# Kernel optimization log

Measured on AMD Instinct MI355X. Metric: run time of the kernel, lower is better.

## Reference

```python
import jax, jax.numpy as jnp
import numpy as np

NEG_FILL = -10000.0  # matches masked_fill_(mask, -10000.0)


def setup_inputs() -> dict:
    key0 = jax.random.key(0)
    kq, kk, kv, km = jax.random.split(key0, 4)
    B, H, S, D = 2, 16, 2048, 64
    query = jax.random.normal(kq, (B, H, S, D), dtype=jnp.float32)
    key = jax.random.normal(kk, (B, H, S, D), dtype=jnp.float32)
    value = jax.random.normal(kv, (B, H, S, D), dtype=jnp.float32)
    # key-padding mask [B, S]; True = position is masked out
    mask = jax.random.randint(km, (B, S), 0, 2).astype(jnp.bool_)
    return {"query": query, "key": key, "value": value, "mask": mask}


def reference(query, key, value, mask):
    # scaled dot-product attention: [B,H,S,D] x [B,H,S,D] -> [B,H,S,S]
    scale = 1.0 / jnp.sqrt(jnp.asarray(query.shape[-1], query.dtype))
    scores = jnp.einsum('bhqd,bhkd->bhqk', query, key) * scale
    # mask [B,S] -> broadcast over heads and query positions as [B,1,1,S]
    scores = jnp.where(mask[:, None, None, :], jnp.asarray(NEG_FILL, scores.dtype), scores)
    attn = jax.nn.softmax(scores, axis=-1)
    # dropout probs are 0 (eval-mode identity)
    out = jnp.einsum('bhqk,bhkd->bhqd', attn, value)
    return out
```

## Files before the change

### kernel.cpp

```cpp
#include <hip/hip_runtime.h>
#include <hip/hip_bf16.h>
#include <stdint.h>

namespace {

constexpr int Bb = 2;
constexpr int Hh = 16;
constexpr int Ss = 2048;
constexpr int Dd = 64;
constexpr int KT = 64;
constexpr int NT = Ss / KT;
constexpr int TILE_BYTES = KT * Dd * 2;
constexpr int BH_BYTES = NT * TILE_BYTES;
constexpr size_t KPRE_BYTES = (size_t)Bb * Hh * Ss * Dd * 2;
constexpr size_t VPRE_OFF = KPRE_BYTES;
constexpr size_t MASK_OFF = 2 * KPRE_BYTES;
constexpr size_t WS_NEED = MASK_OFF + (size_t)Bb * NT * 8;

typedef __bf16 bf16x8 __attribute__((ext_vector_type(8)));
typedef float floatx4 __attribute__((ext_vector_type(4)));

typedef __attribute__((address_space(1))) const unsigned int guint;
typedef __attribute__((address_space(3))) unsigned int luint;

__device__ __forceinline__ void g2lds16(const void* g, void* l) {
  __builtin_amdgcn_global_load_lds((guint*)g, (luint*)l, 16, 0, 0);
}

__global__ __launch_bounds__(256) void preprocess4(
    const float* __restrict__ K, const float* __restrict__ V,
    const int* __restrict__ mask, uint8_t* __restrict__ ws)
{
  const int tid = threadIdx.x;
  const int kt = blockIdx.x;
  const int bh = blockIdx.y;

  if (blockIdx.z == 0) {
    const int c = tid & 7;
#pragma unroll
    for (int half = 0; half < 2; ++half) {
      const int row = (tid >> 3) + half * 32;
      const float4* src = (const float4*)(K + ((size_t)bh * 2048 + kt * 64 + row) * 64 + c * 8);
      const float4 a = src[0], b2 = src[1];
      bf16x8 pk;
      pk[0] = (__bf16)a.x;  pk[1] = (__bf16)a.y;  pk[2] = (__bf16)a.z;  pk[3] = (__bf16)a.w;
      pk[4] = (__bf16)b2.x; pk[5] = (__bf16)b2.y; pk[6] = (__bf16)b2.z; pk[7] = (__bf16)b2.w;
      uint8_t* dst = ws + (size_t)bh * BH_BYTES + kt * TILE_BYTES + row * 128 + ((c ^ (row & 7)) << 4);
      *(bf16x8*)dst = pk;
    }
    if (bh == 0 && kt < 16) {
      const int i = kt * 256 + tid;
      const int bb = i >> 11, key = i & 2047;
      const unsigned long long bal = __ballot(mask[bb * 2048 + key] != 0);
      if ((key & 63) == 0)
        ((unsigned long long*)(ws + MASK_OFF))[bb * NT + (key >> 6)] = bal;
    }
    return;
  }

  const int d2  = tid & 31;
  const int c16 = tid >> 5;
  const int s2 = c16 & 1, q = c16 >> 1;
  const int k0 = 32 * s2 + 4 * q;
  const float* vbase = V + ((size_t)bh * 2048 + kt * 64) * 64;
  float2 col[8];
#pragma unroll
  for (int j = 0; j < 4; ++j) {
    col[j]     = *(const float2*)(vbase + (size_t)(k0 + j) * 64 + 2 * d2);
    col[4 + j] = *(const float2*)(vbase + (size_t)(k0 + 16 + j) * 64 + 2 * d2);
  }
#pragma unroll
  for (int h = 0; h < 2; ++h) {
    const int d = 2 * d2 + h;
    bf16x8 pv;
#pragma unroll
    for (int j = 0; j < 4; ++j) {
      pv[j]     = (__bf16)(h ? col[j].y     : col[j].x);
      pv[4 + j] = (__bf16)(h ? col[4 + j].y : col[4 + j].x);
    }
    uint8_t* dst = ws + VPRE_OFF + (size_t)bh * BH_BYTES + kt * TILE_BYTES + d * 128 + ((c16 ^ (d & 7)) << 4);
    *(bf16x8*)dst = pv;
  }
}

#define NEGM (-14426.950408889634f)
#define MFMA16 __builtin_amdgcn_mfma_f32_16x16x32_bf16

__global__ __launch_bounds__(256, 2) void attn_fused9(
    const float* __restrict__ Q, const uint8_t* __restrict__ ws,
    float* __restrict__ Out)
{
  const int tid  = threadIdx.x;
  const int wave = tid >> 6;
  const int lane = tid & 63;
  const int ln   = lane & 15;
  const int quad = lane >> 4;

  const int bh   = blockIdx.x;
  const int qblk = blockIdx.y;
  const int b    = bh >> 4;

  const float* Qb = Q + (size_t)bh * Ss * Dd;
  float*       Ob = Out + (size_t)bh * Ss * Dd;
  const uint8_t* Kpre = ws + (size_t)bh * BH_BYTES;
  const uint8_t* Vpre = ws + VPRE_OFF + (size_t)bh * BH_BYTES;
  const unsigned long long* Mbits = (const unsigned long long*)(ws + MASK_OFF) + b * NT;

  __shared__ __align__(16) __bf16 Klds[2][64 * Dd];
  __shared__ __align__(16) __bf16 Vlds[2][64 * Dd];

  const int q0A = qblk * 128 + wave * 32;
  const int q0B = q0A + 16;

  const float QS = 0.125f * 1.44269504088896340736f;
  bf16x8 aqA0, aqA1, aqB0, aqB1;
  {
    const float* qpA = Qb + (size_t)(q0A + ln) * Dd + quad * 8;
    const float* qpB = Qb + (size_t)(q0B + ln) * Dd + quad * 8;
#pragma unroll
    for (int j = 0; j < 8; ++j) {
      aqA0[j] = (__bf16)(qpA[j] * QS);
      aqA1[j] = (__bf16)(qpA[32 + j] * QS);
      aqB0[j] = (__bf16)(qpB[j] * QS);
      aqB1[j] = (__bf16)(qpB[32 + j] * QS);
    }
  }

  floatx4 oA[4], oB[4];
  floatx4 laccA = (floatx4){0.f, 0.f, 0.f, 0.f};
  floatx4 laccB = (floatx4){0.f, 0.f, 0.f, 0.f};
#pragma unroll
  for (int nd = 0; nd < 4; ++nd) {
    oA[nd] = (floatx4){0.f, 0.f, 0.f, 0.f};
    oB[nd] = (floatx4){0.f, 0.f, 0.f, 0.f};
  }

  const int swz0 = (quad ^ (ln & 7)) << 4;
  const int swz1 = ((quad + 4) ^ (ln & 7)) << 4;
  const int soff = wave * 1024 + lane * 16;

  g2lds16(Kpre + soff,        (uint8_t*)Klds[0] + soff);
  g2lds16(Kpre + soff + 4096, (uint8_t*)Klds[0] + soff + 4096);
  g2lds16(Vpre + soff,        (uint8_t*)Vlds[0] + soff);
  g2lds16(Vpre + soff + 4096, (uint8_t*)Vlds[0] + soff + 4096);

  for (int it = 0; it < NT; ++it) {
    const int cur = it & 1;
    __syncthreads();

    if (it + 1 < NT) {
      const uint8_t* kg = Kpre + (it + 1) * TILE_BYTES;
      const uint8_t* vg = Vpre + (it + 1) * TILE_BYTES;
      uint8_t* kl = (uint8_t*)Klds[cur ^ 1];
      uint8_t* vl = (uint8_t*)Vlds[cur ^ 1];
      g2lds16(kg + soff,        kl + soff);
      g2lds16(kg + soff + 4096, kl + soff + 4096);
      g2lds16(vg + soff,        vl + soff);
      g2lds16(vg + soff + 4096, vl + soff + 4096);
    }

    const unsigned long long mb = Mbits[it];

    const uint8_t* Kb = (const uint8_t*)Klds[cur];
    const uint8_t* Vb = (const uint8_t*)Vlds[cur];

    auto loadK = [&](int sub, bf16x8& b0, bf16x8& b1) {
      const uint8_t* krow = Kb + (sub * 16 + ln) * 128;
      b0 = *(const bf16x8*)(krow + swz0);
      b1 = *(const bf16x8*)(krow + swz1);
    };
    auto loadV = [&](int s2, bf16x8* w) {
#pragma unroll
      for (int nd = 0; nd < 4; ++nd) {
        const uint8_t* vrow = Vb + (nd * 16 + ln) * 128;
        w[nd] = *(const bf16x8*)(vrow + (((quad * 2 + s2) ^ (ln & 7)) << 4));
      }
    };

    __builtin_amdgcn_s_setprio(1);

    bf16x8 kf0[2][2], kf1[2][2];
    bf16x8 vf[2][4];
    loadK(0, kf0[0][0], kf1[0][0]);
    loadK(1, kf0[0][1], kf1[0][1]);
    loadV(0, vf[0]);

#pragma unroll
    for (int p = 0; p < 2; ++p) {
      if (p == 0) {
        loadK(2, kf0[1][0], kf1[1][0]);
        loadK(3, kf0[1][1], kf1[1][1]);
        loadV(1, vf[1]);
      }

      const uint32_t bits0 = (uint32_t)(mb >> ((2 * p) * 16 + quad * 4));
      const uint32_t bits1 = (uint32_t)(mb >> ((2 * p + 1) * 16 + quad * 4));
      floatx4 sA0, sA1, sB0, sB1;
#pragma unroll
      for (int r = 0; r < 4; ++r) {
        const float b0v = ((bits0 >> r) & 1) ? NEGM : 0.f;
        const float b1v = ((bits1 >> r) & 1) ? NEGM : 0.f;
        sA0[r] = b0v; sB0[r] = b0v;
        sA1[r] = b1v; sB1[r] = b1v;
      }

      sA0 = MFMA16(kf0[p][0], aqA0, sA0, 0, 0, 0);
      sA0 = MFMA16(kf1[p][0], aqA1, sA0, 0, 0, 0);
      sB0 = MFMA16(kf0[p][0], aqB0, sB0, 0, 0, 0);
      sB0 = MFMA16(kf1[p][0], aqB1, sB0, 0, 0, 0);
      sA1 = MFMA16(kf0[p][1], aqA0, sA1, 0, 0, 0);
      sA1 = MFMA16(kf1[p][1], aqA1, sA1, 0, 0, 0);
      sB1 = MFMA16(kf0[p][1], aqB0, sB1, 0, 0, 0);
      sB1 = MFMA16(kf1[p][1], aqB1, sB1, 0, 0, 0);

      bf16x8 bpA, bpB;
#pragma unroll
      for (int r = 0; r < 4; ++r) {
        const float pA0 = __builtin_amdgcn_exp2f(sA0[r]);
        const float pA1 = __builtin_amdgcn_exp2f(sA1[r]);
        const float pB0 = __builtin_amdgcn_exp2f(sB0[r]);
        const float pB1 = __builtin_amdgcn_exp2f(sB1[r]);
        laccA[r] += pA0 + pA1;
        laccB[r] += pB0 + pB1;
        bpA[r] = (__bf16)pA0; bpA[4 + r] = (__bf16)pA1;
        bpB[r] = (__bf16)pB0; bpB[4 + r] = (__bf16)pB1;
      }

#pragma unroll
      for (int nd = 0; nd < 4; ++nd) {
        oA[nd] = MFMA16(vf[p][nd], bpA, oA[nd], 0, 0, 0);
        oB[nd] = MFMA16(vf[p][nd], bpB, oB[nd], 0, 0, 0);
      }
    }
    __builtin_amdgcn_s_setprio(0);
  }

  float lA = (laccA[0] + laccA[1]) + (laccA[2] + laccA[3]);
  float lB = (laccB[0] + laccB[1]) + (laccB[2] + laccB[3]);
  lA += __shfl_xor(lA, 16); lA += __shfl_xor(lA, 32);
  lB += __shfl_xor(lB, 16); lB += __shfl_xor(lB, 32);
  const float iA = 1.0f / lA, iB = 1.0f / lB;
#pragma unroll
  for (int nd = 0; nd < 4; ++nd) {
    float4 wv;
    wv.x = oA[nd][0] * iA; wv.y = oA[nd][1] * iA;
    wv.z = oA[nd][2] * iA; wv.w = oA[nd][3] * iA;
    *(float4*)(Ob + (size_t)(q0A + ln) * Dd + nd * 16 + quad * 4) = wv;
    wv.x = oB[nd][0] * iB; wv.y = oB[nd][1] * iB;
    wv.z = oB[nd][2] * iB; wv.w = oB[nd][3] * iB;
    *(float4*)(Ob + (size_t)(q0B + ln) * Dd + nd * 16 + quad * 4) = wv;
  }
}

}

extern "C" void kernel_launch(void* const* d_in, const int* in_sizes, int n_in,
                              void* d_out, int out_size, void* d_ws, size_t ws_size,
                              hipStream_t stream) {
  const float* Q   = (const float*)d_in[0];
  const float* K   = (const float*)d_in[1];
  const float* V   = (const float*)d_in[2];
  const int*  mask = (const int*)d_in[3];
  float* Out = (float*)d_out;

  preprocess4<<<dim3(32, 32, 2), 256, 0, stream>>>(K, V, mask, (uint8_t*)d_ws);
  attn_fused9<<<dim3(Bb * Hh, Ss / 128), 256, 0, stream>>>(Q, (const uint8_t*)d_ws, Out);
  (void)ws_size; (void)in_sizes; (void)n_in; (void)out_size;
}
```

Measured before the change: 139.0 us.

## Replace LDS double-buffering with direct global-to-register K/V prefetch

Removes the shared-memory staging of K/V tiles and the per-iteration __syncthreads, loading MFMA fragments straight from the pre-swizzled workspace in global memory. The next tile's first-half fragments are prefetched into registers during the second half of the current tile. The aim is to drop barrier and LDS traffic costs so waves run independently. In exchange each wave re-fetches K/V from L2/global, raising cache bandwidth demand and exposing global latency.

```diff
diff --git a/kernel.cpp b/kernel.cpp
--- a/kernel.cpp
+++ b/kernel.cpp
@@ -15,17 +15,9 @@
 constexpr size_t KPRE_BYTES = (size_t)Bb * Hh * Ss * Dd * 2;
 constexpr size_t VPRE_OFF = KPRE_BYTES;
 constexpr size_t MASK_OFF = 2 * KPRE_BYTES;
-constexpr size_t WS_NEED = MASK_OFF + (size_t)Bb * NT * 8;
 
 typedef __bf16 bf16x8 __attribute__((ext_vector_type(8)));
 typedef float floatx4 __attribute__((ext_vector_type(4)));
-
-typedef __attribute__((address_space(1))) const unsigned int guint;
-typedef __attribute__((address_space(3))) unsigned int luint;
-
-__device__ __forceinline__ void g2lds16(const void* g, void* l) {
-  __builtin_amdgcn_global_load_lds((guint*)g, (luint*)l, 16, 0, 0);
-}
 
 __global__ __launch_bounds__(256) void preprocess4(
     const float* __restrict__ K, const float* __restrict__ V,
@@ -86,7 +78,7 @@
 #define NEGM (-14426.950408889634f)
 #define MFMA16 __builtin_amdgcn_mfma_f32_16x16x32_bf16
 
-__global__ __launch_bounds__(256, 2) void attn_fused9(
+__global__ __launch_bounds__(256, 2) void attn_fused10(
     const float* __restrict__ Q, const uint8_t* __restrict__ ws,
     float* __restrict__ Out)
 {
@@ -106,9 +98,6 @@
   const uint8_t* Vpre = ws + VPRE_OFF + (size_t)bh * BH_BYTES;
   const unsigned long long* Mbits = (const unsigned long long*)(ws + MASK_OFF) + b * NT;
 
-  __shared__ __align__(16) __bf16 Klds[2][64 * Dd];
-  __shared__ __align__(16) __bf16 Vlds[2][64 * Dd];
-
   const int q0A = qblk * 128 + wave * 32;
   const int q0B = q0A + 16;
 
@@ -137,60 +126,42 @@
 
   const int swz0 = (quad ^ (ln & 7)) << 4;
   const int swz1 = ((quad + 4) ^ (ln & 7)) << 4;
-  const int soff = wave * 1024 + lane * 16;
-
-  g2lds16(Kpre + soff,        (uint8_t*)Klds[0] + soff);
-  g2lds16(Kpre + soff + 4096, (uint8_t*)Klds[0] + soff + 4096);
-  g2lds16(Vpre + soff,        (uint8_t*)Vlds[0] + soff);
-  g2lds16(Vpre + soff + 4096, (uint8_t*)Vlds[0] + soff + 4096);
+  const int vsw0 = ((quad * 2 + 0) ^ (ln & 7)) << 4;
+  const int vsw1 = ((quad * 2 + 1) ^ (ln & 7)) << 4;
+
+  auto loadK = [&](const uint8_t* Kb, int sub, bf16x8& b0, bf16x8& b1) {
+    const uint8_t* krow = Kb + (sub * 16 + ln) * 128;
+    b0 = *(const bf16x8*)(krow + swz0);
+    b1 = *(const bf16x8*)(krow + swz1);
+  };
+  auto loadV = [&](const uint8_t* Vb, int s2, bf16x8* w) {
+    const int vsw = s2 ? vsw1 : vsw0;
+#pragma unroll
+    for (int nd = 0; nd < 4; ++nd)
+      w[nd] = *(const bf16x8*)(Vb + (nd * 16 + ln) * 128 + vsw);
+  };
+
+  bf16x8 kf0[2][2], kf1[2][2];
+  bf16x8 vf[2][4];
+  loadK(Kpre, 0, kf0[0][0], kf1[0][0]);
+  loadK(Kpre, 1, kf0[0][1], kf1[0][1]);
+  loadV(Vpre, 0, vf[0]);
 
   for (int it = 0; it < NT; ++it) {
-    const int cur = it & 1;
-    __syncthreads();
-
-    if (it + 1 < NT) {
-      const uint8_t* kg = Kpre + (it + 1) * TILE_BYTES;
-      const uint8_t* vg = Vpre + (it + 1) * TILE_BYTES;
-      uint8_t* kl = (uint8_t*)Klds[cur ^ 1];
-      uint8_t* vl = (uint8_t*)Vlds[cur ^ 1];
-      g2lds16(kg + soff,        kl + soff);
-      g2lds16(kg + soff + 4096, kl + soff + 4096);
-      g2lds16(vg + soff,        vl + soff);
-      g2lds16(vg + soff + 4096, vl + soff + 4096);
-    }
-
+    const uint8_t* Kb = Kpre + it * TILE_BYTES;
+    const uint8_t* Vb = Vpre + it * TILE_BYTES;
     const unsigned long long mb = Mbits[it];
-
-    const uint8_t* Kb = (const uint8_t*)Klds[cur];
-    const uint8_t* Vb = (const uint8_t*)Vlds[cur];
-
-    auto loadK = [&](int sub, bf16x8& b0, bf16x8& b1) {
-      const uint8_t* krow = Kb + (sub * 16 + ln) * 128;
-      b0 = *(const bf16x8*)(krow + swz0);
-      b1 = *(const bf16x8*)(krow + swz1);
-    };
-    auto loadV = [&](int s2, bf16x8* w) {
-#pragma unroll
-      for (int nd = 0; nd < 4; ++nd) {
-        const uint8_t* vrow = Vb + (nd * 16 + ln) * 128;
-        w[nd] = *(const bf16x8*)(vrow + (((quad * 2 + s2) ^ (ln & 7)) << 4));
-      }
-    };
-
-    __builtin_amdgcn_s_setprio(1);
-
-    bf16x8 kf0[2][2], kf1[2][2];
-    bf16x8 vf[2][4];
-    loadK(0, kf0[0][0], kf1[0][0]);
-    loadK(1, kf0[0][1], kf1[0][1]);
-    loadV(0, vf[0]);
 
 #pragma unroll
     for (int p = 0; p < 2; ++p) {
       if (p == 0) {
-        loadK(2, kf0[1][0], kf1[1][0]);
-        loadK(3, kf0[1][1], kf1[1][1]);
-        loadV(1, vf[1]);
+        loadK(Kb, 2, kf0[1][0], kf1[1][0]);
+        loadK(Kb, 3, kf0[1][1], kf1[1][1]);
+        loadV(Vb, 1, vf[1]);
+      } else if (it + 1 < NT) {
+        loadK(Kb + TILE_BYTES, 0, kf0[0][0], kf1[0][0]);
+        loadK(Kb + TILE_BYTES, 1, kf0[0][1], kf1[0][1]);
+        loadV(Vb + TILE_BYTES, 0, vf[0]);
       }
 
       const uint32_t bits0 = (uint32_t)(mb >> ((2 * p) * 16 + quad * 4));
@@ -203,6 +174,8 @@
         sA0[r] = b0v; sB0[r] = b0v;
         sA1[r] = b1v; sB1[r] = b1v;
       }
+
+      __builtin_amdgcn_s_setprio(1);
 
       sA0 = MFMA16(kf0[p][0], aqA0, sA0, 0, 0, 0);
       sA0 = MFMA16(kf1[p][0], aqA1, sA0, 0, 0, 0);
@@ -231,8 +204,8 @@
         oA[nd] = MFMA16(vf[p][nd], bpA, oA[nd], 0, 0, 0);
         oB[nd] = MFMA16(vf[p][nd], bpB, oB[nd], 0, 0, 0);
       }
-    }
-    __builtin_amdgcn_s_setprio(0);
+      __builtin_amdgcn_s_setprio(0);
+    }
   }
 
   float lA = (laccA[0] + laccA[1]) + (laccA[2] + laccA[3]);
@@ -264,6 +237,6 @@
   float* Out = (float*)d_out;
 
   preprocess4<<<dim3(32, 32, 2), 256, 0, stream>>>(K, V, mask, (uint8_t*)d_ws);
-  attn_fused9<<<dim3(Bb * Hh, Ss / 128), 256, 0, stream>>>(Q, (const uint8_t*)d_ws, Out);
+  attn_fused10<<<dim3(Bb * Hh, Ss / 128), 256, 0, stream>>>(Q, (const uint8_t*)d_ws, Out);
   (void)ws_size; (void)in_sizes; (void)n_in; (void)out_size;
 }
```

Result: slower. 146.0 us (+5.1%).

## Split attention over two key halves with a separate merge-normalize kernel

Applied to the files above, without the earlier changes.

Adds a split-K path: each block handles half of the key tiles (grid z=2), writes an unnormalized partial output and row sums, and a merge kernel adds the two partials and normalizes. This doubles the block count from 512 to 1024, so more of the GPU's compute units stay busy with a fixed-max softmax that needs no rescaling. The cost is extra global traffic for a second fp32 output buffer and the row sums, plus one more launch. The old single-pass kernel is kept as a fallback when the workspace is too small.

```diff
diff --git a/kernel.cpp b/kernel.cpp
--- a/kernel.cpp
+++ b/kernel.cpp
@@ -15,7 +15,10 @@
 constexpr size_t KPRE_BYTES = (size_t)Bb * Hh * Ss * Dd * 2;
 constexpr size_t VPRE_OFF = KPRE_BYTES;
 constexpr size_t MASK_OFF = 2 * KPRE_BYTES;
-constexpr size_t WS_NEED = MASK_OFF + (size_t)Bb * NT * 8;
+constexpr size_t O1_OFF = MASK_OFF + 1024;
+constexpr size_t O1_BYTES = (size_t)Bb * Hh * Ss * Dd * 4;
+constexpr size_t L_OFF = O1_OFF + O1_BYTES;
+constexpr size_t WS_SPLIT_NEED = L_OFF + 2ull * Bb * Hh * Ss * 4;
 
 typedef __bf16 bf16x8 __attribute__((ext_vector_type(8)));
 typedef float floatx4 __attribute__((ext_vector_type(4)));
@@ -86,7 +89,200 @@
 #define NEGM (-14426.950408889634f)
 #define MFMA16 __builtin_amdgcn_mfma_f32_16x16x32_bf16
 
-__global__ __launch_bounds__(256, 2) void attn_fused9(
+__global__ __launch_bounds__(256, 2) void attn_partial(
+    const float* __restrict__ Q, uint8_t* __restrict__ ws,
+    float* __restrict__ Out)
+{
+  const int tid  = threadIdx.x;
+  const int wave = tid >> 6;
+  const int lane = tid & 63;
+  const int ln   = lane & 15;
+  const int quad = lane >> 4;
+
+  const int bh   = blockIdx.x;
+  const int qblk = blockIdx.y;
+  const int kz   = blockIdx.z;
+  const int b    = bh >> 4;
+
+  const float* Qb = Q + (size_t)bh * Ss * Dd;
+  const uint8_t* Kpre = ws + (size_t)bh * BH_BYTES + (size_t)kz * 16 * TILE_BYTES;
+  const uint8_t* Vpre = ws + VPRE_OFF + (size_t)bh * BH_BYTES + (size_t)kz * 16 * TILE_BYTES;
+  const unsigned long long* Mbits =
+      (const unsigned long long*)(ws + MASK_OFF) + b * NT + kz * 16;
+
+  __shared__ __align__(16) __bf16 Klds[2][64 * Dd];
+  __shared__ __align__(16) __bf16 Vlds[2][64 * Dd];
+
+  const int q0A = qblk * 128 + wave * 32;
+  const int q0B = q0A + 16;
+
+  const float QS = 0.125f * 1.44269504088896340736f;
+  bf16x8 aqA0, aqA1, aqB0, aqB1;
+  {
+    const float* qpA = Qb + (size_t)(q0A + ln) * Dd + quad * 8;
+    const float* qpB = Qb + (size_t)(q0B + ln) * Dd + quad * 8;
+#pragma unroll
+    for (int j = 0; j < 8; ++j) {
+      aqA0[j] = (__bf16)(qpA[j] * QS);
+      aqA1[j] = (__bf16)(qpA[32 + j] * QS);
+      aqB0[j] = (__bf16)(qpB[j] * QS);
+      aqB1[j] = (__bf16)(qpB[32 + j] * QS);
+    }
+  }
+
+  floatx4 oA[4], oB[4];
+  floatx4 laccA = (floatx4){0.f, 0.f, 0.f, 0.f};
+  floatx4 laccB = (floatx4){0.f, 0.f, 0.f, 0.f};
+#pragma unroll
+  for (int nd = 0; nd < 4; ++nd) {
+    oA[nd] = (floatx4){0.f, 0.f, 0.f, 0.f};
+    oB[nd] = (floatx4){0.f, 0.f, 0.f, 0.f};
+  }
+
+  const int swz0 = (quad ^ (ln & 7)) << 4;
+  const int swz1 = ((quad + 4) ^ (ln & 7)) << 4;
+  const int soff = wave * 1024 + lane * 16;
+
+  g2lds16(Kpre + soff,        (uint8_t*)Klds[0] + soff);
+  g2lds16(Kpre + soff + 4096, (uint8_t*)Klds[0] + soff + 4096);
+  g2lds16(Vpre + soff,        (uint8_t*)Vlds[0] + soff);
+  g2lds16(Vpre + soff + 4096, (uint8_t*)Vlds[0] + soff + 4096);
+
+  for (int it = 0; it < 16; ++it) {
+    const int cur = it & 1;
+    __syncthreads();
+
+    if (it + 1 < 16) {
+      const uint8_t* kg = Kpre + (it + 1) * TILE_BYTES;
+      const uint8_t* vg = Vpre + (it + 1) * TILE_BYTES;
+      uint8_t* kl = (uint8_t*)Klds[cur ^ 1];
+      uint8_t* vl = (uint8_t*)Vlds[cur ^ 1];
+      g2lds16(kg + soff,        kl + soff);
+      g2lds16(kg + soff + 4096, kl + soff + 4096);
+      g2lds16(vg + soff,        vl + soff);
+      g2lds16(vg + soff + 4096, vl + soff + 4096);
+    }
+
+    const unsigned long long mb = Mbits[it];
+
+    const uint8_t* Kb = (const uint8_t*)Klds[cur];
+    const uint8_t* Vb = (const uint8_t*)Vlds[cur];
+
+    auto loadK = [&](int sub, bf16x8& b0, bf16x8& b1) {
+      const uint8_t* krow = Kb + (sub * 16 + ln) * 128;
+      b0 = *(const bf16x8*)(krow + swz0);
+      b1 = *(const bf16x8*)(krow + swz1);
+    };
+    auto loadV = [&](int s2, bf16x8* w) {
+#pragma unroll
+      for (int nd = 0; nd < 4; ++nd) {
+        const uint8_t* vrow = Vb + (nd * 16 + ln) * 128;
+        w[nd] = *(const bf16x8*)(vrow + (((quad * 2 + s2) ^ (ln & 7)) << 4));
+      }
+    };
+
+    __builtin_amdgcn_s_setprio(1);
+
+    bf16x8 kf0[2][2], kf1[2][2];
+    bf16x8 vf[2][4];
+    loadK(0, kf0[0][0], kf1[0][0]);
+    loadK(1, kf0[0][1], kf1[0][1]);
+    loadV(0, vf[0]);
+
+#pragma unroll
+    for (int p = 0; p < 2; ++p) {
+      if (p == 0) {
+        loadK(2, kf0[1][0], kf1[1][0]);
+        loadK(3, kf0[1][1], kf1[1][1]);
+        loadV(1, vf[1]);
+      }
+
+      const uint32_t bits0 = (uint32_t)(mb >> ((2 * p) * 16 + quad * 4));
+      const uint32_t bits1 = (uint32_t)(mb >> ((2 * p + 1) * 16 + quad * 4));
+      floatx4 sA0, sA1, sB0, sB1;
+#pragma unroll
+      for (int r = 0; r < 4; ++r) {
+        const float b0v = ((bits0 >> r) & 1) ? NEGM : 0.f;
+        const float b1v = ((bits1 >> r) & 1) ? NEGM : 0.f;
+        sA0[r] = b0v; sB0[r] = b0v;
+        sA1[r] = b1v; sB1[r] = b1v;
+      }
+
+      sA0 = MFMA16(kf0[p][0], aqA0, sA0, 0, 0, 0);
+      sA0 = MFMA16(kf1[p][0], aqA1, sA0, 0, 0, 0);
+      sB0 = MFMA16(kf0[p][0], aqB0, sB0, 0, 0, 0);
+      sB0 = MFMA16(kf1[p][0], aqB1, sB0, 0, 0, 0);
+      sA1 = MFMA16(kf0[p][1], aqA0, sA1, 0, 0, 0);
+      sA1 = MFMA16(kf1[p][1], aqA1, sA1, 0, 0, 0);
+      sB1 = MFMA16(kf0[p][1], aqB0, sB1, 0, 0, 0);
+      sB1 = MFMA16(kf1[p][1], aqB1, sB1, 0, 0, 0);
+
+      bf16x8 bpA, bpB;
+#pragma unroll
+      for (int r = 0; r < 4; ++r) {
+        const float pA0 = __builtin_amdgcn_exp2f(sA0[r]);
+        const float pA1 = __builtin_amdgcn_exp2f(sA1[r]);
+        const float pB0 = __builtin_amdgcn_exp2f(sB0[r]);
+        const float pB1 = __builtin_amdgcn_exp2f(sB1[r]);
+        laccA[r] += pA0 + pA1;
+        laccB[r] += pB0 + pB1;
+        bpA[r] = (__bf16)pA0; bpA[4 + r] = (__bf16)pA1;
+        bpB[r] = (__bf16)pB0; bpB[4 + r] = (__bf16)pB1;
+      }
+
+#pragma unroll
+      for (int nd = 0; nd < 4; ++nd) {
+        oA[nd] = MFMA16(vf[p][nd], bpA, oA[nd], 0, 0, 0);
+        oB[nd] = MFMA16(vf[p][nd], bpB, oB[nd], 0, 0, 0);
+      }
+    }
+    __builtin_amdgcn_s_setprio(0);
+  }
+
+  float lA = (laccA[0] + laccA[1]) + (laccA[2] + laccA[3]);
+  float lB = (laccB[0] + laccB[1]) + (laccB[2] + laccB[3]);
+  lA += __shfl_xor(lA, 16); lA += __shfl_xor(lA, 32);
+  lB += __shfl_xor(lB, 16); lB += __shfl_xor(lB, 32);
+
+  float* Op = (kz == 0) ? Out : (float*)(ws + O1_OFF);
+  Op += (size_t)bh * Ss * Dd;
+#pragma unroll
+  for (int nd = 0; nd < 4; ++nd) {
+    *(float4*)(Op + (size_t)(q0A + ln) * Dd + nd * 16 + quad * 4) =
+        *(const float4*)&oA[nd];
+    *(float4*)(Op + (size_t)(q0B + ln) * Dd + nd * 16 + quad * 4) =
+        *(const float4*)&oB[nd];
+  }
+  float* Lp = (float*)(ws + L_OFF) + (size_t)kz * Bb * Hh * Ss + bh * Ss;
+  if (lane < 16) {
+    Lp[q0A + ln] = lA;
+    Lp[q0B + ln] = lB;
+  }
+}
+
+__global__ __launch_bounds__(256) void merge_norm(
+    float* __restrict__ Out, const uint8_t* __restrict__ ws)
+{
+  const float4* O1 = (const float4*)(ws + O1_OFF);
+  const float* L0 = (const float*)(ws + L_OFF);
+  const float* L1 = L0 + Bb * Hh * Ss;
+  float4* O0 = (float4*)Out;
+  const int total4 = Bb * Hh * Ss * Dd / 4;
+  const int stride = gridDim.x * 256;
+  for (int i = blockIdx.x * 256 + threadIdx.x; i < total4; i += stride) {
+    const int row = i >> 4;
+    const float inv = 1.0f / (L0[row] + L1[row]);
+    float4 a = O0[i];
+    const float4 c = O1[i];
+    a.x = (a.x + c.x) * inv;
+    a.y = (a.y + c.y) * inv;
+    a.z = (a.z + c.z) * inv;
+    a.w = (a.w + c.w) * inv;
+    O0[i] = a;
+  }
+}
+
+__global__ __launch_bounds__(256, 2) void attn_full(
     const float* __restrict__ Q, const uint8_t* __restrict__ ws,
     float* __restrict__ Out)
 {
@@ -160,7 +356,6 @@
     }
 
     const unsigned long long mb = Mbits[it];
-
     const uint8_t* Kb = (const uint8_t*)Klds[cur];
     const uint8_t* Vb = (const uint8_t*)Vlds[cur];
 
@@ -178,7 +373,6 @@
     };
 
     __builtin_amdgcn_s_setprio(1);
-
     bf16x8 kf0[2][2], kf1[2][2];
     bf16x8 vf[2][4];
     loadK(0, kf0[0][0], kf1[0][0]);
@@ -192,7 +386,6 @@
         loadK(3, kf0[1][1], kf1[1][1]);
         loadV(1, vf[1]);
       }
-
       const uint32_t bits0 = (uint32_t)(mb >> ((2 * p) * 16 + quad * 4));
       const uint32_t bits1 = (uint32_t)(mb >> ((2 * p + 1) * 16 + quad * 4));
       floatx4 sA0, sA1, sB0, sB1;
@@ -203,7 +396,6 @@
         sA0[r] = b0v; sB0[r] = b0v;
         sA1[r] = b1v; sB1[r] = b1v;
       }
-
       sA0 = MFMA16(kf0[p][0], aqA0, sA0, 0, 0, 0);
       sA0 = MFMA16(kf1[p][0], aqA1, sA0, 0, 0, 0);
       sB0 = MFMA16(kf0[p][0], aqB0, sB0, 0, 0, 0);
@@ -225,7 +417,6 @@
         bpA[r] = (__bf16)pA0; bpA[4 + r] = (__bf16)pA1;
         bpB[r] = (__bf16)pB0; bpB[4 + r] = (__bf16)pB1;
       }
-
 #pragma unroll
       for (int nd = 0; nd < 4; ++nd) {
         oA[nd] = MFMA16(vf[p][nd], bpA, oA[nd], 0, 0, 0);
@@ -264,6 +455,13 @@
   float* Out = (float*)d_out;
 
   preprocess4<<<dim3(32, 32, 2), 256, 0, stream>>>(K, V, mask, (uint8_t*)d_ws);
-  attn_fused9<<<dim3(Bb * Hh, Ss / 128), 256, 0, stream>>>(Q, (const uint8_t*)d_ws, Out);
-  (void)ws_size; (void)in_sizes; (void)n_in; (void)out_size;
-}
+  if (ws_size >= WS_SPLIT_NEED) {
+    attn_partial<<<dim3(Bb * Hh, Ss / 128, 2), 256, 0, stream>>>(
+        Q, (uint8_t*)d_ws, Out);
+    merge_norm<<<dim3(1024), 256, 0, stream>>>(Out, (const uint8_t*)d_ws);
+  } else {
+    attn_full<<<dim3(Bb * Hh, Ss / 128), 256, 0, stream>>>(
+        Q, (const uint8_t*)d_ws, Out);
+  }
+  (void)in_sizes; (void)n_in; (void)out_size;
+}
```

After: 147.7 us. 6.2% more time.
